# Optimization experiments

Measured on AMD Instinct MI355X. Metric: run time of the kernel, lower is better.

## Reference

```python
import jax, jax.numpy as jnp
import numpy as np
import math

B, L, DF = 1024, 96, 5
D_MODEL, D_FF, N_HEADS = 256, 1024, 8
C_OUT, MA, FACTOR = 5, 25, 3
E_LAYERS, D_LAYERS, EXT = 2, 2, 20


def moving_mean(x, k):
    # torch moving_avg: replicate-pad (k-1)//2 on each side, AvgPool1d(k, stride=1)
    p = (k - 1) // 2
    xp = jnp.concatenate([jnp.repeat(x[:, :1], p, axis=1), x, jnp.repeat(x[:, -1:], p, axis=1)], axis=1)
    cs = jnp.cumsum(xp, axis=1)
    cs = jnp.concatenate([jnp.zeros_like(cs[:, :1]), cs], axis=1)
    return (cs[:, k:] - cs[:, :-k]) / k


def series_decomp(x, k):
    m = moving_mean(x, k)
    return x - m, m


def circ_conv3(x, W):
    # Conv1d(kernel=3, padding=1, padding_mode='circular', bias=False); x (B,T,C), W (O,C,3)
    xp = jnp.pad(x, ((0, 0), (1, 1), (0, 0)), mode='wrap')
    win = jnp.stack([xp[:, :-2], xp[:, 1:-1], xp[:, 2:]], axis=-1)  # (B,T,C,3)
    return jnp.einsum('btct,oct->bto'.replace('btct', 'blct').replace('bto', 'blo'), win, W)


def my_layernorm(x, g, b):
    # LayerNorm over last dim, then subtract per-(batch,channel) seasonal bias (mean over time)
    mu = x.mean(-1, keepdims=True)
    var = ((x - mu) ** 2).mean(-1, keepdims=True)
    xh = (x - mu) / jnp.sqrt(var + 1e-5) * g + b
    return xh - xh.mean(axis=1, keepdims=True)


def time_delay_agg(values, corr):
    # inference-mode time delay aggregation; values, corr: (B,H,E,Lv)
    Bv, H, E, Lv = values.shape
    top_k = int(FACTOR * math.log(Lv))
    mean_value = corr.mean(axis=(1, 2))              # (B,Lv)
    weights, delay = jax.lax.top_k(mean_value, top_k)  # (B,k)
    tmp_corr = jax.nn.softmax(weights, axis=-1)
    ar = jnp.arange(Lv)

    def body(acc, wd):
        w, d = wd                                    # (B,), (B,) int32
        idx = (ar[None, :] + d[:, None]) % Lv        # circular roll == gather on doubled values
        pattern = jnp.take_along_axis(values, idx[:, None, None, :], axis=-1)
        return acc + pattern * w[:, None, None, None], None

    acc, _ = jax.lax.scan(body, jnp.zeros_like(values), (tmp_corr.T, delay.T))
    return acc


def auto_correlation(q, k, v):
    # q (B,Lq,H,E); k,v (B,S,H,E)
    Bq, Lq, H, E = q.shape
    S = v.shape[1]
    if Lq > S:
        pad = jnp.zeros((Bq, Lq - S, H, E), q.dtype)
        k = jnp.concatenate([k, pad], axis=1)
        v = jnp.concatenate([v, pad], axis=1)
    else:
        k, v = k[:, :Lq], v[:, :Lq]
    qf = jnp.fft.rfft(q.transpose(0, 2, 3, 1), axis=-1)
    kf = jnp.fft.rfft(k.transpose(0, 2, 3, 1), axis=-1)
    corr = jnp.fft.irfft(qf * jnp.conj(kf), n=Lq, axis=-1)  # (B,H,E,Lq)
    V = time_delay_agg(v.transpose(0, 2, 3, 1), corr)
    return V.transpose(0, 3, 1, 2)


def ac_layer(xq, xkv, Wq, bq, Wk, bk, Wv, bv, Wo, bo):
    Bq, Lq, _ = xq.shape
    S = xkv.shape[1]
    q = (xq @ Wq.T + bq).reshape(Bq, Lq, N_HEADS, -1)
    k = (xkv @ Wk.T + bk).reshape(Bq, S, N_HEADS, -1)
    v = (xkv @ Wv.T + bv).reshape(Bq, S, N_HEADS, -1)
    V = auto_correlation(q, k, v).reshape(Bq, Lq, -1)
    return V @ Wo.T + bo


def setup_inputs() -> dict:
    ks = iter(jax.random.split(jax.random.key(0), 64))

    def rn(shape, s=0.05):
        return jax.random.normal(next(ks), shape, jnp.float32) * s

    dm, E, D = D_MODEL, E_LAYERS, D_LAYERS
    inp = {'x': jax.random.normal(next(ks), (B, L, DF), jnp.float32)}
    inp['we_enc'] = rn((dm, DF, 3), 0.3)
    inp['we_dec'] = rn((dm, DF, 3), 0.3)
    for w in ('Wq', 'Wk', 'Wv', 'Wo'):
        inp['enc_' + w] = rn((E, dm, dm))
        inp['enc_b' + w[1]] = rn((E, dm))
    inp['enc_W1'] = rn((E, D_FF, dm))
    inp['enc_W2'] = rn((E, dm, D_FF))
    inp['enc_ln_g'] = jnp.ones((dm,), jnp.float32)
    inp['enc_ln_b'] = jnp.zeros((dm,), jnp.float32)
    for p in ('s', 'c'):
        for w in ('Wq', 'Wk', 'Wv', 'Wo'):
            inp['dec_' + p + w] = rn((D, dm, dm))
            inp['dec_' + p + 'b' + w[1]] = rn((D, dm))
    inp['dec_W1'] = rn((D, D_FF, dm))
    inp['dec_W2'] = rn((D, dm, D_FF))
    inp['dec_Wt'] = rn((D, C_OUT, dm, 3), 0.3)
    inp['dec_ln_g'] = jnp.ones((dm,), jnp.float32)
    inp['dec_ln_b'] = jnp.zeros((dm,), jnp.float32)
    inp['proj_W'] = rn((C_OUT, dm), 0.3)
    inp['proj_b'] = jnp.zeros((C_OUT,), jnp.float32)
    inp['bn_g'] = jnp.ones((EXT,), jnp.float32)
    inp['bn_b'] = jnp.zeros((EXT,), jnp.float32)
    inp['bn_rm'] = jnp.zeros((EXT,), jnp.float32)
    inp['bn_rv'] = jnp.ones((EXT,), jnp.float32)
    inp['fc_W'] = rn((1, EXT), 0.3)
    inp['fc_b'] = jnp.zeros((1,), jnp.float32)
    return inp


def reference(x, we_enc, we_dec,
              enc_Wq, enc_bq, enc_Wk, enc_bk, enc_Wv, enc_bv, enc_Wo, enc_bo,
              enc_W1, enc_W2, enc_ln_g, enc_ln_b,
              dec_sWq, dec_sbq, dec_sWk, dec_sbk, dec_sWv, dec_sbv, dec_sWo, dec_sbo,
              dec_cWq, dec_cbq, dec_cWk, dec_cbk, dec_cWv, dec_cbv, dec_cWo, dec_cbo,
              dec_W1, dec_W2, dec_Wt, dec_ln_g, dec_ln_b,
              proj_W, proj_b, bn_g, bn_b, bn_rm, bn_rv, fc_W, fc_b):
    mean = jnp.tile(x.mean(axis=1, keepdims=True), (1, EXT, 1))
    seasonal_init, trend_init = series_decomp(x, MA)
    trend_init = jnp.concatenate([trend_init, mean], axis=1)            # (B, L+EXT, DF)
    seasonal_init = jnp.pad(seasonal_init, ((0, 0), (EXT, 0), (0, 0)))  # 20 zero steps in front
    # encoder
    enc = circ_conv3(x, we_enc)  # DataEmbedding_wo_pos (dropout = identity in eval)
    for i in range(E_LAYERS):
        a = ac_layer(enc, enc, enc_Wq[i], enc_bq[i], enc_Wk[i], enc_bk[i],
                     enc_Wv[i], enc_bv[i], enc_Wo[i], enc_bo[i])
        h, _ = series_decomp(enc + a, MA)
        y = jax.nn.relu(h @ enc_W1[i].T) @ enc_W2[i].T  # 1x1 convs, bias=False
        enc, _ = series_decomp(h + y, MA)
    enc = my_layernorm(enc, enc_ln_g, enc_ln_b)
    # decoder
    dec = circ_conv3(seasonal_init, we_dec)
    trend = trend_init
    for i in range(D_LAYERS):
        a = ac_layer(dec, dec, dec_sWq[i], dec_sbq[i], dec_sWk[i], dec_sbk[i],
                     dec_sWv[i], dec_sbv[i], dec_sWo[i], dec_sbo[i])
        dec, t1 = series_decomp(dec + a, MA)
        a = ac_layer(dec, enc, dec_cWq[i], dec_cbq[i], dec_cWk[i], dec_cbk[i],
                     dec_cWv[i], dec_cbv[i], dec_cWo[i], dec_cbo[i])
        dec, t2 = series_decomp(dec + a, MA)
        y = jax.nn.relu(dec @ dec_W1[i].T) @ dec_W2[i].T
        dec, t3 = series_decomp(dec + y, MA)
        trend = trend + circ_conv3(t1 + t2 + t3, dec_Wt[i])
    dec = my_layernorm(dec, dec_ln_g, dec_ln_b)
    seasonal = dec @ proj_W.T + proj_b          # (B, L+EXT, C_OUT)
    seasonal = jnp.tile(seasonal, (1, 1, 4))    # (B, L+EXT, 20)
    out = jnp.tile(trend, (1, 1, 4)) + seasonal  # trend tiled to 20 channels (see notes)
    last = out[:, -1, :]                         # (B, 20)
    h = (last - bn_rm) / jnp.sqrt(bn_rv + 1e-5) * bn_g + bn_b  # BatchNorm1d eval
    return (h @ fc_W.T + fc_b)[:, 0]
```

## Files before the change

kernel.cpp:

```cpp
#include <hip/hip_runtime.h>
#include <hip/hip_bf16.h>
#include <cstdint>
#include <cstddef>

#define B_   1024
#define LE   96
#define LD   116
#define DM   256
#define DFF  1024

typedef __attribute__((ext_vector_type(8))) short bf16x8;
typedef __attribute__((ext_vector_type(4))) float f32x4;

static __device__ __forceinline__ unsigned short f2b(float f) {
  __hip_bfloat16 h = __float2bfloat16(f);
  return *reinterpret_cast<unsigned short*>(&h);
}
static __device__ __forceinline__ float asf(unsigned int u) { return __uint_as_float(u); }
static __device__ __forceinline__ void split1(float f, unsigned short& h, unsigned short& l) {
  h = f2b(f);
  l = f2b(f - asf((unsigned int)h << 16));
}
static __device__ __forceinline__ unsigned int pck(float f) {
  unsigned short h, l; split1(f, h, l);
  return ((unsigned int)h << 16) | l;
}
static __device__ __forceinline__ float unp(unsigned int p) {
  return asf(p & 0xFFFF0000u) + asf(p << 16);
}
static __device__ __forceinline__ void split8(float4 a, float4 b, uint4& h4, uint4& l4) {
  float f[8] = {a.x, a.y, a.z, a.w, b.x, b.y, b.z, b.w};
  unsigned int hp[4], lp[4];
#pragma unroll
  for (int j = 0; j < 4; ++j) {
    unsigned short h0, l0, h1, l1;
    split1(f[2 * j], h0, l0);
    split1(f[2 * j + 1], h1, l1);
    hp[j] = (unsigned int)h0 | ((unsigned int)h1 << 16);
    lp[j] = (unsigned int)l0 | ((unsigned int)l1 << 16);
  }
  h4 = make_uint4(hp[0], hp[1], hp[2], hp[3]);
  l4 = make_uint4(lp[0], lp[1], lp[2], lp[3]);
}
static __device__ __forceinline__ void unpack8(uint4 a, uint4 b, uint4& h, uint4& l) {
  h.x = (a.y & 0xFFFF0000u) | (a.x >> 16);
  l.x = (a.y << 16) | (a.x & 0xFFFFu);
  h.y = (a.w & 0xFFFF0000u) | (a.z >> 16);
  l.y = (a.w << 16) | (a.z & 0xFFFFu);
  h.z = (b.y & 0xFFFF0000u) | (b.x >> 16);
  l.z = (b.y << 16) | (b.x & 0xFFFFu);
  h.w = (b.w & 0xFFFF0000u) | (b.z >> 16);
  l.w = (b.w << 16) | (b.z & 0xFFFFu);
}

typedef const __attribute__((address_space(1))) void* gas_ptr;
typedef __attribute__((address_space(3))) void* las_ptr;
static __device__ __forceinline__ void gload16(const void* g, void* l) {
  __builtin_amdgcn_global_load_lds((gas_ptr)g, (las_ptr)l, 16, 0, 0);
}

#define NE_ ((size_t)B_ * LE * DM)
#define ND_ ((size_t)B_ * LD * DM)
#define NS_ ((size_t)B_ * LD * 5)
#define NW_ ((size_t)B_ * 16)
#define HID_ ((size_t)29696 * DFF)
#define WBF_ 3670016

static constexpr size_t o_enc   = 0;
static constexpr size_t o_dec   = o_enc   + NE_ * 4;
static constexpr size_t o_q     = o_dec   + ND_ * 4;
static constexpr size_t o_kbuf  = o_q     + ND_ * 4;
static constexpr size_t o_qkvp  = o_kbuf  + ND_ * 4;
static constexpr size_t o_qxp   = o_qkvp  + ND_ * 12;
static constexpr size_t o_ench  = o_qxp   + ND_ * 4;
static constexpr size_t o_encl  = o_ench  + NE_ * 2;
static constexpr size_t o_dech  = o_encl  + NE_ * 2;
static constexpr size_t o_decl  = o_dech  + ND_ * 2;
static constexpr size_t o_gthh  = o_decl  + ND_ * 2;
static constexpr size_t o_gthl  = o_gthh  + ND_ * 2;
static constexpr size_t o_hidp  = o_gthl  + ND_ * 2;
static constexpr size_t o_spad  = o_hidp  + HID_ * 4;
static constexpr size_t o_trend = o_spad  + NS_ * 4;
static constexpr size_t o_wtop  = o_trend + NS_ * 4;
static constexpr size_t o_dtop  = o_wtop  + NW_ * 4;
static constexpr size_t o_bias  = o_dtop  + NW_ * 4;
static constexpr size_t o_whi   = o_bias  + 6 * 768 * 4;
static constexpr size_t o_wlo   = o_whi   + (size_t)WBF_ * 2;
static constexpr size_t WS_TOTAL = o_wlo  + (size_t)WBF_ * 2;

__device__ __align__(256) unsigned char g_ws[WS_TOTAL];

static __host__ __device__ constexpr size_t enc_base(int i) { return (size_t)i * 786432; }
static __host__ __device__ constexpr size_t dec_base(int i) { return 1572864 + (size_t)i * 1048576; }

__global__ __launch_bounds__(256)
void k_cast_split(const float* __restrict__ in, unsigned short* __restrict__ hi,
                  unsigned short* __restrict__ lo, int n) {
  int i = (blockIdx.x * 256 + threadIdx.x) * 4;
  if (i < n) {
    float4 v = *(const float4*)(in + i);
    unsigned int hp[2], lp[2];
    float f[4] = {v.x, v.y, v.z, v.w};
#pragma unroll
    for (int j = 0; j < 2; ++j) {
      unsigned short h0, l0, h1, l1;
      split1(f[2 * j], h0, l0);
      split1(f[2 * j + 1], h1, l1);
      hp[j] = (unsigned int)h0 | ((unsigned int)h1 << 16);
      lp[j] = (unsigned int)l0 | ((unsigned int)l1 << 16);
    }
    *(uint2*)(hi + i) = make_uint2(hp[0], hp[1]);
    *(uint2*)(lo + i) = make_uint2(lp[0], lp[1]);
  }
}

__global__ __launch_bounds__(256)
void k_cat3(const float* __restrict__ a, const float* __restrict__ b,
            const float* __restrict__ c, float* __restrict__ dst) {
  int t = threadIdx.x;
  dst[t] = a[t];
  dst[256 + t] = b[t];
  if (c) dst[512 + t] = c[t];
}

__global__ __launch_bounds__(128)
void k_pre(const float* __restrict__ x, float* __restrict__ spad, float* __restrict__ trend) {
  int b = blockIdx.x;
  __shared__ float xs[LE * 5];
  __shared__ float mx[5];
  const float* xb = x + (size_t)b * LE * 5;
  for (int i = threadIdx.x; i < LE * 5; i += 128) xs[i] = xb[i];
  __syncthreads();
  if (threadIdx.x < 5) {
    float s = 0.f;
    for (int t = 0; t < LE; ++t) s += xs[t * 5 + threadIdx.x];
    mx[threadIdx.x] = s * (1.f / 96.f);
  }
  __syncthreads();
  float* spb = spad + (size_t)b * LD * 5;
  float* trb = trend + (size_t)b * LD * 5;
  for (int i = threadIdx.x; i < LE * 5; i += 128) {
    int t = i / 5, c = i % 5;
    float s = 0.f;
    for (int d = -12; d <= 12; ++d) {
      int tt = t + d; tt = tt < 0 ? 0 : (tt > LE - 1 ? LE - 1 : tt);
      s += xs[tt * 5 + c];
    }
    float m = s * (1.f / 25.f);
    trb[t * 5 + c] = m;
    spb[(t + 20) * 5 + c] = xs[i] - m;
  }
  for (int i = threadIdx.x; i < 20 * 5; i += 128) {
    int t = i / 5, c = i % 5;
    spb[t * 5 + c] = 0.f;
    trb[(LE + t) * 5 + c] = mx[c];
  }
}

__global__ __launch_bounds__(256)
void k_conv3(const float* __restrict__ xin, const float* __restrict__ W,
             float* __restrict__ out, unsigned short* __restrict__ ohi,
             unsigned short* __restrict__ olo, int L) {
  int b = blockIdx.x, o = threadIdx.x;
  __shared__ float xs[LD * 5];
  const float* xb = xin + (size_t)b * L * 5;
  for (int i = o; i < L * 5; i += 256) xs[i] = xb[i];
  __syncthreads();
  float w[15];
#pragma unroll
  for (int j = 0; j < 15; ++j) w[j] = W[o * 15 + j];
  size_t ob = (size_t)b * L * DM + o;
  for (int l = 0; l < L; ++l) {
    int lm = (l == 0) ? L - 1 : l - 1;
    int lp = (l == L - 1) ? 0 : l + 1;
    float acc = 0.f;
#pragma unroll
    for (int c = 0; c < 5; ++c)
      acc += xs[lm * 5 + c] * w[c * 3] + xs[l * 5 + c] * w[c * 3 + 1] + xs[lp * 5 + c] * w[c * 3 + 2];
    size_t gi = ob + (size_t)l * DM;
    out[gi] = acc;
    unsigned short h, lo2; split1(acc, h, lo2);
    ohi[gi] = h; olo[gi] = lo2;
  }
}

template <int XMODE, int OMODE, bool RELU>
__global__ __launch_bounds__(256)
void k_gemm_ps(const unsigned short* __restrict__ Xhi, const unsigned short* __restrict__ Xlo,
               const unsigned int* __restrict__ Xp,
               const unsigned short* __restrict__ Whi, const unsigned short* __restrict__ Wlo,
               const float* __restrict__ bias, float* __restrict__ Cf,
               unsigned int* __restrict__ Cp, int M, int N, int K) {
  __shared__ __align__(16) unsigned short Xh[4096], Xl[4096], Wh[4096], Wl[4096];
  const int nwg = gridDim.x, bid = blockIdx.x;
  const int wg = (bid & 7) * (nwg >> 3) + (bid >> 3);
  const int NT = N >> 7;
  const int mt = wg / NT, nt = wg % NT;
  const int m0 = mt << 7, n0 = nt << 7;
  const int tid = threadIdx.x, lane = tid & 63, wv = tid >> 6;
  const int wm = (wv >> 1) << 6, wn = (wv & 1) << 6;

  f32x4 acc[4][4];
#pragma unroll
  for (int i = 0; i < 4; ++i)
#pragma unroll
    for (int j = 0; j < 4; ++j) acc[i][j] = (f32x4){0.f, 0.f, 0.f, 0.f};

  const int r0 = tid >> 2,        ls0 = (tid & 3) ^ ((r0 >> 1) & 3);
  const int r1 = 64 + (tid >> 2), ls1 = (tid & 3) ^ ((r1 >> 1) & 3);
  const unsigned short* wh0 = Whi + (size_t)(n0 + r0) * K + (ls0 << 3);
  const unsigned short* wh1 = Whi + (size_t)(n0 + r1) * K + (ls1 << 3);
  const unsigned short* wl0 = Wlo + (size_t)(n0 + r0) * K + (ls0 << 3);
  const unsigned short* wl1 = Wlo + (size_t)(n0 + r1) * K + (ls1 << 3);
  const int lofs0 = (tid & ~63) << 3, lofs1 = 2048 + ((tid & ~63) << 3);

  const unsigned short* xh0 = nullptr; const unsigned short* xh1 = nullptr;
  const unsigned short* xl0 = nullptr; const unsigned short* xl1 = nullptr;
  const unsigned int* xp0 = nullptr; const unsigned int* xp1 = nullptr;
  unsigned short *xh0d = nullptr, *xl0d = nullptr, *xh1d = nullptr, *xl1d = nullptr;
  if (XMODE == 0) {
    xh0 = Xhi + (size_t)(m0 + r0) * K + (ls0 << 3);
    xh1 = Xhi + (size_t)(m0 + r1) * K + (ls1 << 3);
    xl0 = Xlo + (size_t)(m0 + r0) * K + (ls0 << 3);
    xl1 = Xlo + (size_t)(m0 + r1) * K + (ls1 << 3);
  } else {
    const int xrow0 = tid >> 2, xpart = tid & 3;
    const int xrow1 = 64 + xrow0;
    xp0 = Xp + (size_t)(m0 + xrow0) * K + (xpart << 3);
    xp1 = Xp + (size_t)(m0 + xrow1) * K + (xpart << 3);
    const int xph0 = xpart ^ ((xrow0 >> 1) & 3);
    const int xph1 = xpart ^ ((xrow1 >> 1) & 3);
    xh0d = Xh + xrow0 * 32 + (xph0 << 3);
    xl0d = Xl + xrow0 * 32 + (xph0 << 3);
    xh1d = Xh + xrow1 * 32 + (xph1 << 3);
    xl1d = Xl + xrow1 * 32 + (xph1 << 3);
  }

  for (int k0 = 0; k0 < K; k0 += 32) {
    gload16(wh0 + k0, Wh + lofs0);
    gload16(wh1 + k0, Wh + lofs1);
    gload16(wl0 + k0, Wl + lofs0);
    gload16(wl1 + k0, Wl + lofs1);
    if (XMODE == 0) {
      gload16(xh0 + k0, Xh + lofs0);
      gload16(xh1 + k0, Xh + lofs1);
      gload16(xl0 + k0, Xl + lofs0);
      gload16(xl1 + k0, Xl + lofs1);
    } else {
      uint4 a0 = *(const uint4*)(xp0 + k0);
      uint4 b0 = *(const uint4*)(xp0 + k0 + 4);
      uint4 a1 = *(const uint4*)(xp1 + k0);
      uint4 b1 = *(const uint4*)(xp1 + k0 + 4);
      uint4 h, l;
      unpack8(a0, b0, h, l);
      *(uint4*)xh0d = h; *(uint4*)xl0d = l;
      unpack8(a1, b1, h, l);
      *(uint4*)xh1d = h; *(uint4*)xl1d = l;
    }
    __syncthreads();
    bf16x8 ah[4], al[4], bh[4], bl[4];
#pragma unroll
    for (int i = 0; i < 4; ++i) {
      int ra = wm + i * 16 + (lane & 15);
      int sa = (lane >> 4) ^ ((ra >> 1) & 3);
      ah[i] = *(const bf16x8*)(Xh + ra * 32 + (sa << 3));
      al[i] = *(const bf16x8*)(Xl + ra * 32 + (sa << 3));
      int rb = wn + i * 16 + (lane & 15);
      int sb = (lane >> 4) ^ ((rb >> 1) & 3);
      bh[i] = *(const bf16x8*)(Wh + rb * 32 + (sb << 3));
      bl[i] = *(const bf16x8*)(Wl + rb * 32 + (sb << 3));
    }
#pragma unroll
    for (int i = 0; i < 4; ++i)
#pragma unroll
      for (int j = 0; j < 4; ++j) {
        acc[i][j] = __builtin_amdgcn_mfma_f32_16x16x32_bf16(ah[i], bh[j], acc[i][j], 0, 0, 0);
        acc[i][j] = __builtin_amdgcn_mfma_f32_16x16x32_bf16(al[i], bh[j], acc[i][j], 0, 0, 0);
        acc[i][j] = __builtin_amdgcn_mfma_f32_16x16x32_bf16(ah[i], bl[j], acc[i][j], 0, 0, 0);
      }
    __syncthreads();
  }
// ... 109 lines not shown

  float* vals = (float*)smem;
  float* rv   = vals + 128;
  int*   ri   = (int*)(rv + 128);
  float* selv = (float*)(ri + 128);
  int*   seli = (int*)(selv + 16);
  if (tid < 128) vals[tid] = (tid < L) ? s : -3e38f;
  __syncthreads();
  for (int it = 0; it < TK; ++it) {
    if (tid < 128) { rv[tid] = vals[tid]; ri[tid] = tid; }
    __syncthreads();
    for (int off = 64; off >= 1; off >>= 1) {
      if (tid < off) {
        float v2 = rv[tid + off]; int i2 = ri[tid + off];
        if (v2 > rv[tid] || (v2 == rv[tid] && i2 < ri[tid])) { rv[tid] = v2; ri[tid] = i2; }
      }
      __syncthreads();
    }
    if (tid == 0) { selv[it] = rv[0]; seli[it] = ri[0]; vals[ri[0]] = -3e38f; }
    __syncthreads();
  }
  if (tid == 0) {
    float mxv = selv[0];
    float e[16]; float sum = 0.f;
    for (int j = 0; j < TK; ++j) { e[j] = expf(selv[j] - mxv); sum += e[j]; }
    float inv = 1.f / sum;
    for (int j = 0; j < TK; ++j) {
      wout[(size_t)b * 16 + j] = e[j] * inv;
      dout[(size_t)b * 16 + j] = seli[j];
    }
  }
}

__global__ __launch_bounds__(256)
void k_gather4(const unsigned int* __restrict__ V, int sv, const float* __restrict__ wtop,
               const int* __restrict__ dtop, unsigned short* __restrict__ ohi,
               unsigned short* __restrict__ olo, int L, int S, int TK, int G8) {
  int p = blockIdx.x;
  int xcd = p & 7, q8 = p >> 3;
  int lg = q8 % G8;
  int b = ((q8 / G8) << 3) + xcd;
  __shared__ float wsm[16];
  __shared__ int   dsm[16];
  if (threadIdx.x < TK) {
    wsm[threadIdx.x] = wtop[(size_t)b * 16 + threadIdx.x];
    dsm[threadIdx.x] = dtop[(size_t)b * 16 + threadIdx.x];
  }
  __syncthreads();
  int wv = threadIdx.x >> 6, lane = threadIdx.x & 63;
  int c4 = lane << 2;
  const unsigned int* Vb = V + (size_t)b * S * sv + c4;
  size_t ob = (size_t)b * L * DM + c4;
#pragma unroll
  for (int u = 0; u < 2; ++u) {
    int l = (lg << 3) + (wv << 1) + u;
    if (l < L) {
      float a0 = 0.f, a1 = 0.f, a2 = 0.f, a3 = 0.f;
      for (int j = 0; j < TK; ++j) {
        int r = l + dsm[j]; if (r >= L) r -= L;
        if (r < S) {
          uint4 v = *(const uint4*)(Vb + (size_t)r * sv);
          float w = wsm[j];
          a0 += w * unp(v.x); a1 += w * unp(v.y); a2 += w * unp(v.z); a3 += w * unp(v.w);
        }
      }
      unsigned short h0, l0, h1, l1, h2, l2, h3, l3;
      split1(a0, h0, l0); split1(a1, h1, l1); split1(a2, h2, l2); split1(a3, h3, l3);
      uint2 hp, lp;
      hp.x = (unsigned int)h0 | ((unsigned int)h1 << 16);
      hp.y = (unsigned int)h2 | ((unsigned int)h3 << 16);
      lp.x = (unsigned int)l0 | ((unsigned int)l1 << 16);
      lp.y = (unsigned int)l2 | ((unsigned int)l3 << 16);
      *(uint2*)(ohi + ob + (size_t)l * DM) = hp;
      *(uint2*)(olo + ob + (size_t)l * DM) = lp;
    }
  }
}

template <int MOUT>
__global__ __launch_bounds__(128)
void k_decomp(const float* __restrict__ X, const float* __restrict__ Y,
              float* __restrict__ out, unsigned short* __restrict__ ohi,
              unsigned short* __restrict__ olo, float* __restrict__ mout, int L) {
  int b = blockIdx.x >> 2, qd = blockIdx.x & 3;
  __shared__ float tmp[LD * 64];
  size_t base = (size_t)b * L * DM + qd * 64;
  for (int i = threadIdx.x; i < L * 64; i += 128) {
    int t = i >> 6, cc = i & 63;
    size_t gi = base + (size_t)t * DM + cc;
    tmp[i] = X[gi] + Y[gi];
  }
  __syncthreads();
  int c = threadIdx.x & 63, th = threadIdx.x >> 6;
  int half = L >> 1;
  int t0 = th * half, t1 = t0 + half;
  float s = 0.f;
  for (int d = -12; d <= 12; ++d) {
    int t2 = t0 + d; t2 = t2 < 0 ? 0 : (t2 > L - 1 ? L - 1 : t2);
    s += tmp[t2 * 64 + c];
  }
  for (int t = t0; t < t1; ++t) {
    float m = s * (1.f / 25.f);
    size_t gi = base + (size_t)t * DM + c;
    float o = tmp[t * 64 + c] - m;
    out[gi] = o;
    unsigned short h, l; split1(o, h, l);
    ohi[gi] = h; olo[gi] = l;
    if (MOUT) mout[gi] = m;
    int ai = t + 13; if (ai > L - 1) ai = L - 1;
    int si = t - 12; if (si < 0) si = 0;
    s += tmp[ai * 64 + c] - tmp[si * 64 + c];
  }
}

__global__ __launch_bounds__(256)
void k_lnorm(const float* __restrict__ X, const float* __restrict__ g,
             float* __restrict__ out, unsigned short* __restrict__ ohi,
             unsigned short* __restrict__ olo, int L) {
  int b = blockIdx.x;
  __shared__ float mu_s[LD], inv_s[LD];
  size_t base = (size_t)b * L * DM;
  int wv = threadIdx.x >> 6, lane = threadIdx.x & 63;
  for (int t = wv; t < L; t += 4) {
    float s = 0.f, s2 = 0.f;
#pragma unroll
    for (int qd = 0; qd < 4; ++qd) {
      float val = X[base + (size_t)t * DM + lane + 64 * qd];
      s += val; s2 += val * val;
    }
    for (int off = 32; off; off >>= 1) { s += __shfl_xor(s, off); s2 += __shfl_xor(s2, off); }
    if (lane == 0) {
      float mu = s * (1.f / 256.f);
      mu_s[t] = mu;
      inv_s[t] = rsqrtf(s2 * (1.f / 256.f) - mu * mu + 1e-5f);
    }
  }
  __syncthreads();
  int c = threadIdx.x;
  float gc = g[c];
  float sm = 0.f;
  for (int t = 0; t < L; ++t) sm += (X[base + (size_t)t * DM + c] - mu_s[t]) * inv_s[t];
  float mn = sm / (float)L;
  for (int t = 0; t < L; ++t) {
    float xn = (X[base + (size_t)t * DM + c] - mu_s[t]) * inv_s[t];
    float o = gc * (xn - mn);
    size_t gi = base + (size_t)t * DM + c;
    out[gi] = o;
    unsigned short h, l; split1(o, h, l);
    ohi[gi] = h; olo[gi] = l;
  }
}

__global__ __launch_bounds__(256)
void k_trendconv(const float* __restrict__ T, const float* __restrict__ Wt,
                 float* __restrict__ trend, int L) {
  int b = blockIdx.x;
  int tid = threadIdx.x, wv = tid >> 6, lane = tid & 63;
  int c0 = lane << 2;
  float w[5][3][4];
#pragma unroll
  for (int o = 0; o < 5; ++o)
#pragma unroll
    for (int k = 0; k < 4; ++k) {
      w[o][0][k] = Wt[o * 768 + (c0 + k) * 3 + 0];
      w[o][1][k] = Wt[o * 768 + (c0 + k) * 3 + 1];
      w[o][2][k] = Wt[o * 768 + (c0 + k) * 3 + 2];
    }
  size_t base = (size_t)b * L * DM;
  int chunk = (L + 3) >> 2;
  int l0 = wv * chunk;
  int cnt = (L - l0 < chunk) ? (L - l0) : chunk;
  if (cnt <= 0) return;
  int lmi = (l0 == 0) ? L - 1 : l0 - 1;
  float4 pm = *(const float4*)(T + base + (size_t)lmi * DM + c0);
  float4 p0 = *(const float4*)(T + base + (size_t)l0  * DM + c0);
  for (int i = 0; i < cnt; ++i) {
    int l = l0 + i;
    int lp = (l == L - 1) ? 0 : l + 1;
    float4 pp = *(const float4*)(T + base + (size_t)lp * DM + c0);
    float fm[4] = {pm.x, pm.y, pm.z, pm.w};
    float f0[4] = {p0.x, p0.y, p0.z, p0.w};
    float fp[4] = {pp.x, pp.y, pp.z, pp.w};
// ... 63 lines not shown
  const float* enc_bk = (const float*)d_in[6];
  const float* enc_Wv = (const float*)d_in[7];
  const float* enc_bv = (const float*)d_in[8];
  const float* enc_Wo = (const float*)d_in[9];
  const float* enc_bo = (const float*)d_in[10];
  const float* enc_W1 = (const float*)d_in[11];
  const float* enc_W2 = (const float*)d_in[12];
  const float* enc_g  = (const float*)d_in[13];
  const float* sWq = (const float*)d_in[15]; const float* sbq = (const float*)d_in[16];
  const float* sWk = (const float*)d_in[17]; const float* sbk = (const float*)d_in[18];
  const float* sWv = (const float*)d_in[19]; const float* sbv = (const float*)d_in[20];
  const float* sWo = (const float*)d_in[21]; const float* sbo = (const float*)d_in[22];
  const float* cWq = (const float*)d_in[23]; const float* cbq = (const float*)d_in[24];
  const float* cWk = (const float*)d_in[25]; const float* cbk = (const float*)d_in[26];
  const float* cWv = (const float*)d_in[27]; const float* cbv = (const float*)d_in[28];
  const float* cWo = (const float*)d_in[29]; const float* cbo = (const float*)d_in[30];
  const float* dW1 = (const float*)d_in[31]; const float* dW2 = (const float*)d_in[32];
  const float* dWt = (const float*)d_in[33];
  const float* dec_g  = (const float*)d_in[34];
  const float* projW = (const float*)d_in[36]; const float* projb = (const float*)d_in[37];
  const float* bng = (const float*)d_in[38]; const float* bnb = (const float*)d_in[39];
  const float* bnrm = (const float*)d_in[40]; const float* bnrv = (const float*)d_in[41];
  const float* fcW = (const float*)d_in[42]; const float* fcb = (const float*)d_in[43];
  (void)in_sizes; (void)n_in; (void)out_size; (void)d_ws; (void)ws_size;
  float* outp = (float*)d_out;

  void* symaddr = nullptr;
  if (hipGetSymbolAddress(&symaddr, HIP_SYMBOL(g_ws)) != hipSuccess || !symaddr) return;
  unsigned char* base = (unsigned char*)symaddr;
  float* enc   = (float*)(base + o_enc);
  float* dec   = (float*)(base + o_dec);
  float* q     = (float*)(base + o_q);
  float* kbuf  = (float*)(base + o_kbuf);
  unsigned int* qkvp = (unsigned int*)(base + o_qkvp);
  unsigned int* qxp  = (unsigned int*)(base + o_qxp);
  unsigned short* ench = (unsigned short*)(base + o_ench);
  unsigned short* encl = (unsigned short*)(base + o_encl);
  unsigned short* dech = (unsigned short*)(base + o_dech);
  unsigned short* decl = (unsigned short*)(base + o_decl);
  unsigned short* gthh = (unsigned short*)(base + o_gthh);
  unsigned short* gthl = (unsigned short*)(base + o_gthl);
  unsigned int*   hidp = (unsigned int*)(base + o_hidp);
  float* spad  = (float*)(base + o_spad);
  float* trend = (float*)(base + o_trend);
  float* wtop  = (float*)(base + o_wtop);
  int*   dtop  = (int*)(base + o_dtop);
  float* biasb = (float*)(base + o_bias);
  unsigned short* whi = (unsigned short*)(base + o_whi);
  unsigned short* wlo = (unsigned short*)(base + o_wlo);

  const int ME = B_ * LE;
  const int MD = B_ * LD;

  auto cast = [&](const float* s, size_t off, int n) {
    k_cast_split<<<n / 1024, 256, 0, stream>>>(s, whi + off, wlo + off, n);
  };
  for (int i = 0; i < 2; ++i) {
    size_t e = enc_base(i), d = dec_base(i);
    size_t wq = (size_t)i * 65536, wf = (size_t)i * 262144;
    cast(enc_Wq + wq, e + 0, 65536);       cast(enc_Wk + wq, e + 65536, 65536);
    cast(enc_Wv + wq, e + 131072, 65536);  cast(enc_Wo + wq, e + 196608, 65536);
    cast(enc_W1 + wf, e + 262144, 262144); cast(enc_W2 + wf, e + 524288, 262144);
    cast(sWq + wq, d + 0, 65536);          cast(sWk + wq, d + 65536, 65536);
    cast(sWv + wq, d + 131072, 65536);     cast(sWo + wq, d + 196608, 65536);
    cast(cWq + wq, d + 262144, 65536);     cast(cWk + wq, d + 327680, 65536);
    cast(cWv + wq, d + 393216, 65536);     cast(cWo + wq, d + 458752, 65536);
    cast(dW1 + wf, d + 524288, 262144);    cast(dW2 + wf, d + 786432, 262144);
    size_t b_ = (size_t)i * DM;
    k_cat3<<<1, 256, 0, stream>>>(enc_bq + b_, enc_bk + b_, enc_bv + b_, biasb + (size_t)i * 768);
    k_cat3<<<1, 256, 0, stream>>>(sbq + b_, sbk + b_, sbv + b_, biasb + (size_t)(2 + i) * 768);
    k_cat3<<<1, 256, 0, stream>>>(cbk + b_, cbv + b_, nullptr, biasb + (size_t)(4 + i) * 768);
  }

  auto gemm_f = [&](const unsigned short* Xh, const unsigned short* Xl, size_t woff,
                    const float* bias, float* Cf, int M, int N, int K) {
    int nwg = (M >> 7) * (N >> 7);
    k_gemm_ps<0, 0, false><<<nwg, 256, 0, stream>>>(Xh, Xl, nullptr, whi + woff, wlo + woff,
                                                    bias, Cf, nullptr, M, N, K);
  };
  auto gemm_p = [&](const unsigned short* Xh, const unsigned short* Xl, size_t woff,
                    const float* bias, unsigned int* Cp, int M, int N, int K) {
    int nwg = (M >> 7) * (N >> 7);
    k_gemm_ps<0, 1, false><<<nwg, 256, 0, stream>>>(Xh, Xl, nullptr, whi + woff, wlo + woff,
                                                    bias, nullptr, Cp, M, N, K);
  };
  auto ffn = [&](const unsigned short* srch, const unsigned short* srcl, int M,
                 size_t w1, size_t w2) {
    int done = 0;
    while (done < M) {
      int mc = (M - done < 29696) ? (M - done) : 29696;
      int nwg1 = (mc >> 7) * (DFF >> 7);
      k_gemm_ps<0, 1, true><<<nwg1, 256, 0, stream>>>(srch + (size_t)done * DM,
                                                      srcl + (size_t)done * DM, nullptr,
                                                      whi + w1, wlo + w1, nullptr,
                                                      nullptr, hidp, mc, DFF, DM);
      int nwg2 = (mc >> 7) * (DM >> 7);
      k_gemm_ps<1, 0, false><<<nwg2, 256, 0, stream>>>(nullptr, nullptr, hidp,
                                                       whi + w2, wlo + w2, nullptr,
                                                       kbuf + (size_t)done * DM, nullptr,
                                                       mc, DM, DFF);
      done += mc;
    }
  };
  auto attn_self = [&](const unsigned short* srch, const unsigned short* srcl, int Lq,
                       size_t wqkv, size_t wo2, const float* biasr, const float* bo, int TK) {
    int M = B_ * Lq;
    int G8 = (Lq + 7) >> 3;
    gemm_p(srch, srcl, wqkv, biasr, qkvp, M, 768, DM);
    k_corr_split<<<B_, 256, 0, stream>>>(qkvp, 768, qkvp + 256, 768, wtop, dtop, Lq, Lq, TK);
    k_gather4<<<B_ * G8, 256, 0, stream>>>(qkvp + 512, 768, wtop, dtop, gthh, gthl, Lq, Lq, TK, G8);
    gemm_f(gthh, gthl, wo2, bo, q, M, DM, DM);
  };
  auto attn_cross = [&](size_t wq2, size_t wkv, size_t wo2, const float* bq,
                        const float* biasr, const float* bo, int TK) {
    int G8 = (LD + 7) >> 3;
    gemm_p(dech, decl, wq2, bq, qxp, MD, DM, DM);
    gemm_p(ench, encl, wkv, biasr, qkvp, ME, 512, DM);
    k_corr_split<<<B_, 256, 0, stream>>>(qxp, 256, qkvp, 512, wtop, dtop, LD, LE, TK);
    k_gather4<<<B_ * G8, 256, 0, stream>>>(qkvp + 256, 512, wtop, dtop, gthh, gthl, LD, LE, TK, G8);
    gemm_f(gthh, gthl, wo2, bo, q, MD, DM, DM);
  };

  k_pre<<<B_, 128, 0, stream>>>(x, spad, trend);
  k_conv3<<<B_, 256, 0, stream>>>(x, we_enc, enc, ench, encl, LE);
  k_conv3<<<B_, 256, 0, stream>>>(spad, we_dec, dec, dech, decl, LD);

  for (int i = 0; i < 2; ++i) {
    size_t e = enc_base(i), b_ = (size_t)i * DM;
    attn_self(ench, encl, LE, e + 0, e + 196608, biasb + (size_t)i * 768, enc_bo + b_, 13);
    k_decomp<0><<<4 * B_, 128, 0, stream>>>(enc, q, enc, ench, encl, nullptr, LE);
    ffn(ench, encl, ME, e + 262144, e + 524288);
    k_decomp<0><<<4 * B_, 128, 0, stream>>>(enc, kbuf, enc, ench, encl, nullptr, LE);
  }
  k_lnorm<<<B_, 256, 0, stream>>>(enc, enc_g, enc, ench, encl, LE);

  for (int i = 0; i < 2; ++i) {
    size_t d = dec_base(i), b_ = (size_t)i * DM;
    const float* Wt_i = dWt + (size_t)i * 5 * DM * 3;
    attn_self(dech, decl, LD, d + 0, d + 196608, biasb + (size_t)(2 + i) * 768, sbo + b_, 14);
    k_decomp<1><<<4 * B_, 128, 0, stream>>>(dec, q, dec, dech, decl, kbuf, LD);
    k_trendconv<<<B_, 256, 0, stream>>>(kbuf, Wt_i, trend, LD);
    attn_cross(d + 262144, d + 327680, d + 458752, cbq + b_, biasb + (size_t)(4 + i) * 768, cbo + b_, 14);
    k_decomp<1><<<4 * B_, 128, 0, stream>>>(dec, q, dec, dech, decl, kbuf, LD);
    k_trendconv<<<B_, 256, 0, stream>>>(kbuf, Wt_i, trend, LD);
    ffn(dech, decl, MD, d + 524288, d + 786432);
    k_decomp<1><<<4 * B_, 128, 0, stream>>>(dec, kbuf, dec, dech, decl, q, LD);
    k_trendconv<<<B_, 256, 0, stream>>>(q, Wt_i, trend, LD);
  }
  k_lnorm<<<B_, 256, 0, stream>>>(dec, dec_g, dec, dech, decl, LD);

  k_final<<<B_, 256, 0, stream>>>(dec, trend, projW, projb, bng, bnb, bnrm, bnrv, fcW, fcb, outp);
}
```

Baseline: 6.477 ms.

## Fold Wq·Wk and Wo·Wv into composed weights for self-attention, pack activations

For self-attention, correlation is computed from X·(WkᵀWq) against the raw input, and the value path uses a precomposed Wo·Wv, so the separate Q/K projection and output GEMM are dropped; the gather writes the final float output with a folded bias. Activations are stored as packed hi/lo uint32 everywhere instead of separate hi/lo arrays, so the GEMM has a single input mode. The FFN hidden buffer is enlarged so it runs unchunked. Dropping the Q/K biases and composing the weights in split-bf16 changes rounding and relies on the correlation being bilinear in Q and K.

```diff
diff --git a/kernel.cpp b/kernel.cpp
--- a/kernel.cpp
+++ b/kernel.cpp
@@ -27,20 +27,6 @@
 }
 static __device__ __forceinline__ float unp(unsigned int p) {
   return asf(p & 0xFFFF0000u) + asf(p << 16);
-}
-static __device__ __forceinline__ void split8(float4 a, float4 b, uint4& h4, uint4& l4) {
-  float f[8] = {a.x, a.y, a.z, a.w, b.x, b.y, b.z, b.w};
-  unsigned int hp[4], lp[4];
-#pragma unroll
-  for (int j = 0; j < 4; ++j) {
-    unsigned short h0, l0, h1, l1;
-    split1(f[2 * j], h0, l0);
-    split1(f[2 * j + 1], h1, l1);
-    hp[j] = (unsigned int)h0 | ((unsigned int)h1 << 16);
-    lp[j] = (unsigned int)l0 | ((unsigned int)l1 << 16);
-  }
-  h4 = make_uint4(hp[0], hp[1], hp[2], hp[3]);
-  l4 = make_uint4(lp[0], lp[1], lp[2], lp[3]);
 }
 static __device__ __forceinline__ void unpack8(uint4 a, uint4 b, uint4& h, uint4& l) {
   h.x = (a.y & 0xFFFF0000u) | (a.x >> 16);
@@ -63,35 +49,31 @@
 #define ND_ ((size_t)B_ * LD * DM)
 #define NS_ ((size_t)B_ * LD * 5)
 #define NW_ ((size_t)B_ * 16)
-#define HID_ ((size_t)29696 * DFF)
-#define WBF_ 3670016
+#define WBF_ 3145728
 
 static constexpr size_t o_enc   = 0;
 static constexpr size_t o_dec   = o_enc   + NE_ * 4;
 static constexpr size_t o_q     = o_dec   + ND_ * 4;
 static constexpr size_t o_kbuf  = o_q     + ND_ * 4;
-static constexpr size_t o_qkvp  = o_kbuf  + ND_ * 4;
-static constexpr size_t o_qxp   = o_qkvp  + ND_ * 12;
-static constexpr size_t o_ench  = o_qxp   + ND_ * 4;
-static constexpr size_t o_encl  = o_ench  + NE_ * 2;
-static constexpr size_t o_dech  = o_encl  + NE_ * 2;
-static constexpr size_t o_decl  = o_dech  + ND_ * 2;
-static constexpr size_t o_gthh  = o_decl  + ND_ * 2;
-static constexpr size_t o_gthl  = o_gthh  + ND_ * 2;
-static constexpr size_t o_hidp  = o_gthl  + ND_ * 2;
-static constexpr size_t o_spad  = o_hidp  + HID_ * 4;
+static constexpr size_t o_yup   = o_kbuf  + ND_ * 4;
+static constexpr size_t o_qxp   = o_yup   + ND_ * 8;
+static constexpr size_t o_encp  = o_qxp   + ND_ * 4;
+static constexpr size_t o_decp  = o_encp  + NE_ * 4;
+static constexpr size_t o_gthp  = o_decp  + ND_ * 4;
+static constexpr size_t o_hidp  = o_gthp  + ND_ * 4;
+static constexpr size_t o_spad  = o_hidp  + ND_ * 16;
 static constexpr size_t o_trend = o_spad  + NS_ * 4;
 static constexpr size_t o_wtop  = o_trend + NS_ * 4;
 static constexpr size_t o_dtop  = o_wtop  + NW_ * 4;
 static constexpr size_t o_bias  = o_dtop  + NW_ * 4;
-static constexpr size_t o_whi   = o_bias  + 6 * 768 * 4;
+static constexpr size_t o_whi   = o_bias  + 2048 * 4;
 static constexpr size_t o_wlo   = o_whi   + (size_t)WBF_ * 2;
 static constexpr size_t WS_TOTAL = o_wlo  + (size_t)WBF_ * 2;
 
 __device__ __align__(256) unsigned char g_ws[WS_TOTAL];
 
-static __host__ __device__ constexpr size_t enc_base(int i) { return (size_t)i * 786432; }
-static __host__ __device__ constexpr size_t dec_base(int i) { return 1572864 + (size_t)i * 1048576; }
+static __host__ __device__ constexpr size_t enc_base(int i) { return (size_t)i * 655360; }
+static __host__ __device__ constexpr size_t dec_base(int i) { return 1310720 + (size_t)i * 917504; }
 
 __global__ __launch_bounds__(256)
 void k_cast_split(const float* __restrict__ in, unsigned short* __restrict__ hi,
@@ -115,12 +97,46 @@
 }
 
 __global__ __launch_bounds__(256)
-void k_cat3(const float* __restrict__ a, const float* __restrict__ b,
-            const float* __restrict__ c, float* __restrict__ dst) {
+void k_compose_qk(const float* __restrict__ Wq, const float* __restrict__ Wk,
+                  unsigned short* __restrict__ hi, unsigned short* __restrict__ lo) {
+  int j = blockIdx.x, i = threadIdx.x;
+  __shared__ float wkc[256];
+  wkc[i] = Wk[i * 256 + j];
+  __syncthreads();
+  float s = 0.f;
+  for (int o = 0; o < 256; ++o) s += Wq[o * 256 + i] * wkc[o];
+  unsigned short h, l; split1(s, h, l);
+  hi[j * 256 + i] = h; lo[j * 256 + i] = l;
+}
+__global__ __launch_bounds__(256)
+void k_compose_vo(const float* __restrict__ Wv, const float* __restrict__ Wo,
+                  unsigned short* __restrict__ hi, unsigned short* __restrict__ lo) {
+  int o2 = blockIdx.x, i = threadIdx.x;
+  __shared__ float woc[256];
+  woc[i] = Wo[o2 * 256 + i];
+  __syncthreads();
+  float s = 0.f;
+  for (int c = 0; c < 256; ++c) s += woc[c] * Wv[c * 256 + i];
+  unsigned short h, l; split1(s, h, l);
+  hi[o2 * 256 + i] = h; lo[o2 * 256 + i] = l;
+}
+__global__ __launch_bounds__(256)
+void k_bout(const float* __restrict__ Wo, const float* __restrict__ bv,
+            const float* __restrict__ bo, float* __restrict__ dst) {
+  int o2 = threadIdx.x;
+  __shared__ float bvs[256];
+  bvs[o2] = bv[o2];
+  __syncthreads();
+  float s = bo[o2];
+  for (int c = 0; c < 256; ++c) s += Wo[o2 * 256 + c] * bvs[c];
+  dst[o2] = s;
+}
+
+__global__ __launch_bounds__(256)
+void k_cat2(const float* __restrict__ a, const float* __restrict__ b, float* __restrict__ dst) {
   int t = threadIdx.x;
   dst[t] = a[t];
   dst[256 + t] = b[t];
-  if (c) dst[512 + t] = c[t];
 }
 
 __global__ __launch_bounds__(128)
@@ -159,8 +175,7 @@
 
 __global__ __launch_bounds__(256)
 void k_conv3(const float* __restrict__ xin, const float* __restrict__ W,
-             float* __restrict__ out, unsigned short* __restrict__ ohi,
-             unsigned short* __restrict__ olo, int L) {
+             float* __restrict__ out, unsigned int* __restrict__ shp, int L) {
   int b = blockIdx.x, o = threadIdx.x;
   __shared__ float xs[LD * 5];
   const float* xb = xin + (size_t)b * L * 5;
@@ -179,15 +194,13 @@
       acc += xs[lm * 5 + c] * w[c * 3] + xs[l * 5 + c] * w[c * 3 + 1] + xs[lp * 5 + c] * w[c * 3 + 2];
     size_t gi = ob + (size_t)l * DM;
     out[gi] = acc;
-    unsigned short h, lo2; split1(acc, h, lo2);
-    ohi[gi] = h; olo[gi] = lo2;
-  }
-}
-
-template <int XMODE, int OMODE, bool RELU>
-__global__ __launch_bounds__(256)
-void k_gemm_ps(const unsigned short* __restrict__ Xhi, const unsigned short* __restrict__ Xlo,
-               const unsigned int* __restrict__ Xp,
+    shp[gi] = pck(acc);
+  }
+}
+
+template <int OMODE, bool RELU>
+__global__ __launch_bounds__(256)
+void k_gemm_pk(const unsigned int* __restrict__ Xp,
                const unsigned short* __restrict__ Whi, const unsigned short* __restrict__ Wlo,
                const float* __restrict__ bias, float* __restrict__ Cf,
                unsigned int* __restrict__ Cp, int M, int N, int K) {
@@ -214,39 +227,23 @@
   const unsigned short* wl1 = Wlo + (size_t)(n0 + r1) * K + (ls1 << 3);
   const int lofs0 = (tid & ~63) << 3, lofs1 = 2048 + ((tid & ~63) << 3);
 
-  const unsigned short* xh0 = nullptr; const unsigned short* xh1 = nullptr;
-  const unsigned short* xl0 = nullptr; const unsigned short* xl1 = nullptr;
-  const unsigned int* xp0 = nullptr; const unsigned int* xp1 = nullptr;
-  unsigned short *xh0d = nullptr, *xl0d = nullptr, *xh1d = nullptr, *xl1d = nullptr;
-  if (XMODE == 0) {
-    xh0 = Xhi + (size_t)(m0 + r0) * K + (ls0 << 3);
-    xh1 = Xhi + (size_t)(m0 + r1) * K + (ls1 << 3);
-    xl0 = Xlo + (size_t)(m0 + r0) * K + (ls0 << 3);
-    xl1 = Xlo + (size_t)(m0 + r1) * K + (ls1 << 3);
-  } else {
-    const int xrow0 = tid >> 2, xpart = tid & 3;
-    const int xrow1 = 64 + xrow0;
-    xp0 = Xp + (size_t)(m0 + xrow0) * K + (xpart << 3);
-    xp1 = Xp + (size_t)(m0 + xrow1) * K + (xpart << 3);
-    const int xph0 = xpart ^ ((xrow0 >> 1) & 3);
-    const int xph1 = xpart ^ ((xrow1 >> 1) & 3);
-    xh0d = Xh + xrow0 * 32 + (xph0 << 3);
-    xl0d = Xl + xrow0 * 32 + (xph0 << 3);
-    xh1d = Xh + xrow1 * 32 + (xph1 << 3);
-    xl1d = Xl + xrow1 * 32 + (xph1 << 3);
-  }
+  const int xrow0 = tid >> 2, xpart = tid & 3;
+  const int xrow1 = 64 + xrow0;
+  const unsigned int* xp0 = Xp + (size_t)(m0 + xrow0) * K + (xpart << 3);
+  const unsigned int* xp1 = Xp + (size_t)(m0 + xrow1) * K + (xpart << 3);
+  const int xph0 = xpart ^ ((xrow0 >> 1) & 3);
+  const int xph1 = xpart ^ ((xrow1 >> 1) & 3);
+  unsigned short* xh0d = Xh + xrow0 * 32 + (xph0 << 3);
+  unsigned short* xl0d = Xl + xrow0 * 32 + (xph0 << 3);
+  unsigned short* xh1d = Xh + xrow1 * 32 + (xph1 << 3);
+  unsigned short* xl1d = Xl + xrow1 * 32 + (xph1 << 3);
 
   for (int k0 = 0; k0 < K; k0 += 32) {
     gload16(wh0 + k0, Wh + lofs0);
     gload16(wh1 + k0, Wh + lofs1);
     gload16(wl0 + k0, Wl + lofs0);
     gload16(wl1 + k0, Wl + lofs1);
-    if (XMODE == 0) {
-      gload16(xh0 + k0, Xh + lofs0);
-      gload16(xh1 + k0, Xh + lofs1);
-      gload16(xl0 + k0, Xl + lofs0);
-      gload16(xl1 + k0, Xl + lofs1);
-    } else {
+    {
       uint4 a0 = *(const uint4*)(xp0 + k0);
       uint4 b0 = *(const uint4*)(xp0 + k0 + 4);
       uint4 a1 = *(const uint4*)(xp1 + k0);
@@ -422,20 +419,24 @@
   }
 }
 
-__global__ __launch_bounds__(256)
-void k_gather4(const unsigned int* __restrict__ V, int sv, const float* __restrict__ wtop,
-               const int* __restrict__ dtop, unsigned short* __restrict__ ohi,
-               unsigned short* __restrict__ olo, int L, int S, int TK, int G8) {
+template <int SELF>
+__global__ __launch_bounds__(256)
+void k_gather5(const unsigned int* __restrict__ V, int sv, const float* __restrict__ wtop,
+               const int* __restrict__ dtop, float* __restrict__ outf,
+               unsigned int* __restrict__ outp, const float* __restrict__ bout,
+               int L, int S, int TK, int G8) {
   int p = blockIdx.x;
   int xcd = p & 7, q8 = p >> 3;
   int lg = q8 % G8;
   int b = ((q8 / G8) << 3) + xcd;
   __shared__ float wsm[16];
   __shared__ int   dsm[16];
+  __shared__ float bsm[256];
   if (threadIdx.x < TK) {
     wsm[threadIdx.x] = wtop[(size_t)b * 16 + threadIdx.x];
     dsm[threadIdx.x] = dtop[(size_t)b * 16 + threadIdx.x];
   }
+  if (SELF) bsm[threadIdx.x] = bout[threadIdx.x];
   __syncthreads();
   int wv = threadIdx.x >> 6, lane = threadIdx.x & 63;
   int c4 = lane << 2;
@@ -454,15 +455,15 @@
           a0 += w * unp(v.x); a1 += w * unp(v.y); a2 += w * unp(v.z); a3 += w * unp(v.w);
         }
       }
-      unsigned short h0, l0, h1, l1, h2, l2, h3, l3;
-      split1(a0, h0, l0); split1(a1, h1, l1); split1(a2, h2, l2); split1(a3, h3, l3);
-      uint2 hp, lp;
-      hp.x = (unsigned int)h0 | ((unsigned int)h1 << 16);
-      hp.y = (unsigned int)h2 | ((unsigned int)h3 << 16);
-      lp.x = (unsigned int)l0 | ((unsigned int)l1 << 16);
-      lp.y = (unsigned int)l2 | ((unsigned int)l3 << 16);
-      *(uint2*)(ohi + ob + (size_t)l * DM) = hp;
-      *(uint2*)(olo + ob + (size_t)l * DM) = lp;
+      if (SELF) {
+        float4 o;
+        o.x = a0 + bsm[c4];     o.y = a1 + bsm[c4 + 1];
+        o.z = a2 + bsm[c4 + 2]; o.w = a3 + bsm[c4 + 3];
+        *(float4*)(outf + ob + (size_t)l * DM) = o;
+      } else {
+        uint4 o; o.x = pck(a0); o.y = pck(a1); o.z = pck(a2); o.w = pck(a3);
+        *(uint4*)(outp + ob + (size_t)l * DM) = o;
+      }
     }
   }
 }
@@ -470,8 +471,8 @@
 template <int MOUT>
 __global__ __launch_bounds__(128)
 void k_decomp(const float* __restrict__ X, const float* __restrict__ Y,
-              float* __restrict__ out, unsigned short* __restrict__ ohi,
-              unsigned short* __restrict__ olo, float* __restrict__ mout, int L) {
+              float* __restrict__ out, unsigned int* __restrict__ shp,
+              float* __restrict__ mout, int L) {
   int b = blockIdx.x >> 2, qd = blockIdx.x & 3;
   __shared__ float tmp[LD * 64];
   size_t base = (size_t)b * L * DM + qd * 64;
@@ -494,8 +495,7 @@
     size_t gi = base + (size_t)t * DM + c;
     float o = tmp[t * 64 + c] - m;
     out[gi] = o;
-    unsigned short h, l; split1(o, h, l);
-    ohi[gi] = h; olo[gi] = l;
+    shp[gi] = pck(o);
     if (MOUT) mout[gi] = m;
     int ai = t + 13; if (ai > L - 1) ai = L - 1;
     int si = t - 12; if (si < 0) si = 0;
@@ -505,8 +505,7 @@
 
 __global__ __launch_bounds__(256)
 void k_lnorm(const float* __restrict__ X, const float* __restrict__ g,
-             float* __restrict__ out, unsigned short* __restrict__ ohi,
-             unsigned short* __restrict__ olo, int L) {
+             float* __restrict__ out, unsigned int* __restrict__ shp, int L) {
   int b = blockIdx.x;
   __shared__ float mu_s[LD], inv_s[LD];
   size_t base = (size_t)b * L * DM;
@@ -536,8 +535,7 @@
     float o = gc * (xn - mn);
     size_t gi = base + (size_t)t * DM + c;
     out[gi] = o;
-    unsigned short h, l; split1(o, h, l);
-    ohi[gi] = h; olo[gi] = l;
+    shp[gi] = pck(o);
   }
 }
 
@@ -667,15 +665,12 @@
   float* dec   = (float*)(base + o_dec);
   float* q     = (float*)(base + o_q);
   float* kbuf  = (float*)(base + o_kbuf);
-  unsigned int* qkvp = (unsigned int*)(base + o_qkvp);
+  unsigned int* yup  = (unsigned int*)(base + o_yup);
   unsigned int* qxp  = (unsigned int*)(base + o_qxp);
-  unsigned short* ench = (unsigned short*)(base + o_ench);
-  unsigned short* encl = (unsigned short*)(base + o_encl);
-  unsigned short* dech = (unsigned short*)(base + o_dech);
-  unsigned short* decl = (unsigned short*)(base + o_decl);
-  unsigned short* gthh = (unsigned short*)(base + o_gthh);
-  unsigned short* gthl = (unsigned short*)(base + o_gthl);
-  unsigned int*   hidp = (unsigned int*)(base + o_hidp);
+  unsigned int* encp = (unsigned int*)(base + o_encp);
+  unsigned int* decp = (unsigned int*)(base + o_decp);
+  unsigned int* gthp = (unsigned int*)(base + o_gthp);
+  unsigned int* hidp = (unsigned int*)(base + o_hidp);
   float* spad  = (float*)(base + o_spad);
   float* trend = (float*)(base + o_trend);
   float* wtop  = (float*)(base + o_wtop);
@@ -693,96 +688,84 @@
   for (int i = 0; i < 2; ++i) {
     size_t e = enc_base(i), d = dec_base(i);
     size_t wq = (size_t)i * 65536, wf = (size_t)i * 262144;
-    cast(enc_Wq + wq, e + 0, 65536);       cast(enc_Wk + wq, e + 65536, 65536);
-    cast(enc_Wv + wq, e + 131072, 65536);  cast(enc_Wo + wq, e + 196608, 65536);
-    cast(enc_W1 + wf, e + 262144, 262144); cast(enc_W2 + wf, e + 524288, 262144);
-    cast(sWq + wq, d + 0, 65536);          cast(sWk + wq, d + 65536, 65536);
-    cast(sWv + wq, d + 131072, 65536);     cast(sWo + wq, d + 196608, 65536);
-    cast(cWq + wq, d + 262144, 65536);     cast(cWk + wq, d + 327680, 65536);
-    cast(cWv + wq, d + 393216, 65536);     cast(cWo + wq, d + 458752, 65536);
-    cast(dW1 + wf, d + 524288, 262144);    cast(dW2 + wf, d + 786432, 262144);
     size_t b_ = (size_t)i * DM;
-    k_cat3<<<1, 256, 0, stream>>>(enc_bq + b_, enc_bk + b_, enc_bv + b_, biasb + (size_t)i * 768);
-    k_cat3<<<1, 256, 0, stream>>>(sbq + b_, sbk + b_, sbv + b_, biasb + (size_t)(2 + i) * 768);
-    k_cat3<<<1, 256, 0, stream>>>(cbk + b_, cbv + b_, nullptr, biasb + (size_t)(4 + i) * 768);
-  }
-
-  auto gemm_f = [&](const unsigned short* Xh, const unsigned short* Xl, size_t woff,
-                    const float* bias, float* Cf, int M, int N, int K) {
+    k_compose_qk<<<256, 256, 0, stream>>>(enc_Wq + wq, enc_Wk + wq, whi + e, wlo + e);
+    k_compose_vo<<<256, 256, 0, stream>>>(enc_Wv + wq, enc_Wo + wq, whi + e + 65536, wlo + e + 65536);
+    k_bout<<<1, 256, 0, stream>>>(enc_Wo + wq, enc_bv + b_, enc_bo + b_, biasb + (size_t)i * 256);
+    cast(enc_W1 + wf, e + 131072, 262144);
+    cast(enc_W2 + wf, e + 393216, 262144);
+    k_compose_qk<<<256, 256, 0, stream>>>(sWq + wq, sWk + wq, whi + d, wlo + d);
+    k_compose_vo<<<256, 256, 0, stream>>>(sWv + wq, sWo + wq, whi + d + 65536, wlo + d + 65536);
+    k_bout<<<1, 256, 0, stream>>>(sWo + wq, sbv + b_, sbo + b_, biasb + (size_t)(2 + i) * 256);
+    cast(cWq + wq, d + 131072, 65536);
+    cast(cWk + wq, d + 196608, 65536);
+    cast(cWv + wq, d + 262144, 65536);
+    cast(cWo + wq, d + 327680, 65536);
+    cast(dW1 + wf, d + 393216, 262144);
+    cast(dW2 + wf, d + 655360, 262144);
+    k_cat2<<<1, 256, 0, stream>>>(cbk + b_, cbv + b_, biasb + 1024 + (size_t)i * 512);
+  }
+
+  auto gemm_f = [&](const unsigned int* Xp, size_t woff, const float* bias, float* Cf,
+                    int M, int N, int K) {
     int nwg = (M >> 7) * (N >> 7);
-    k_gemm_ps<0, 0, false><<<nwg, 256, 0, stream>>>(Xh, Xl, nullptr, whi + woff, wlo + woff,
-                                                    bias, Cf, nullptr, M, N, K);
+    k_gemm_pk<0, false><<<nwg, 256, 0, stream>>>(Xp, whi + woff, wlo + woff, bias, Cf, nullptr, M, N, K);
   };
-  auto gemm_p = [&](const unsigned short* Xh, const unsigned short* Xl, size_t woff,
-                    const float* bias, unsigned int* Cp, int M, int N, int K) {
+  auto gemm_p = [&](const unsigned int* Xp, size_t woff, const float* bias, unsigned int* Cp,
+                    int M, int N, int K, bool relu) {
     int nwg = (M >> 7) * (N >> 7);
-    k_gemm_ps<0, 1, false><<<nwg, 256, 0, stream>>>(Xh, Xl, nullptr, whi + woff, wlo + woff,
-                                                    bias, nullptr, Cp, M, N, K);
+    if (relu) k_gemm_pk<1, true ><<<nwg, 256, 0, stream>>>(Xp, whi + woff, wlo + woff, bias, nullptr, Cp, M, N, K);
+    else      k_gemm_pk<1, false><<<nwg, 256, 0, stream>>>(Xp, whi + woff, wlo + woff, bias, nullptr, Cp, M, N, K);
   };
-  auto ffn = [&](const unsigned short* srch, const unsigned short* srcl, int M,
-                 size_t w1, size_t w2) {
-    int done = 0;
-    while (done < M) {
-      int mc = (M - done < 29696) ? (M - done) : 29696;
-      int nwg1 = (mc >> 7) * (DFF >> 7);
-      k_gemm_ps<0, 1, true><<<nwg1, 256, 0, stream>>>(srch + (size_t)done * DM,
-                                                      srcl + (size_t)done * DM, nullptr,
-                                                      whi + w1, wlo + w1, nullptr,
-                                                      nullptr, hidp, mc, DFF, DM);
-      int nwg2 = (mc >> 7) * (DM >> 7);
-      k_gemm_ps<1, 0, false><<<nwg2, 256, 0, stream>>>(nullptr, nullptr, hidp,
-                                                       whi + w2, wlo + w2, nullptr,
-                                                       kbuf + (size_t)done * DM, nullptr,
-                                                       mc, DM, DFF);
-      done += mc;
-    }
+  auto ffn = [&](const unsigned int* srcp, int M, size_t w1, size_t w2) {
+    gemm_p(srcp, w1, nullptr, hidp, M, DFF, DM, true);
+    gemm_f(hidp, w2, nullptr, kbuf, M, DM, DFF);
   };
-  auto attn_self = [&](const unsigned short* srch, const unsigned short* srcl, int Lq,
-                       size_t wqkv, size_t wo2, const float* biasr, const float* bo, int TK) {
+  auto attn_self = [&](const unsigned int* srcp, int Lq, size_t wyu, const float* bout, int TK) {
     int M = B_ * Lq;
     int G8 = (Lq + 7) >> 3;
-    gemm_p(srch, srcl, wqkv, biasr, qkvp, M, 768, DM);
-    k_corr_split<<<B_, 256, 0, stream>>>(qkvp, 768, qkvp + 256, 768, wtop, dtop, Lq, Lq, TK);
-    k_gather4<<<B_ * G8, 256, 0, stream>>>(qkvp + 512, 768, wtop, dtop, gthh, gthl, Lq, Lq, TK, G8);
-    gemm_f(gthh, gthl, wo2, bo, q, M, DM, DM);
+    gemm_p(srcp, wyu, nullptr, yup, M, 512, DM, false);
+    k_corr_split<<<B_, 256, 0, stream>>>(yup, 512, srcp, 256, wtop, dtop, Lq, Lq, TK);
+    k_gather5<1><<<B_ * G8, 256, 0, stream>>>(yup + 256, 512, wtop, dtop, q, nullptr, bout, Lq, Lq, TK, G8);
   };
   auto attn_cross = [&](size_t wq2, size_t wkv, size_t wo2, const float* bq,
-                        const float* biasr, const float* bo, int TK) {
+                        const float* bkv, const float* bo, int TK) {
     int G8 = (LD + 7) >> 3;
-    gemm_p(dech, decl, wq2, bq, qxp, MD, DM, DM);
-    gemm_p(ench, encl, wkv, biasr, qkvp, ME, 512, DM);
-    k_corr_split<<<B_, 256, 0, stream>>>(qxp, 256, qkvp, 512, wtop, dtop, LD, LE, TK);
-    k_gather4<<<B_ * G8, 256, 0, stream>>>(qkvp + 256, 512, wtop, dtop, gthh, gthl, LD, LE, TK, G8);
-    gemm_f(gthh, gthl, wo2, bo, q, MD, DM, DM);
+    gemm_p(decp, wq2, bq, qxp, MD, DM, DM, false);
+    gemm_p(encp, wkv, bkv, yup, ME, 512, DM, false);
+    k_corr_split<<<B_, 256, 0, stream>>>(qxp, 256, yup, 512, wtop, dtop, LD, LE, TK);
+    k_gather5<0><<<B_ * G8, 256, 0, stream>>>(yup + 256, 512, wtop, dtop, nullptr, gthp, nullptr, LD, LE, TK, G8);
+    gemm_f(gthp, wo2, bo, q, MD, DM, DM);
   };
 
   k_pre<<<B_, 128, 0, stream>>>(x, spad, trend);
-  k_conv3<<<B_, 256, 0, stream>>>(x, we_enc, enc, ench, encl, LE);
-  k_conv3<<<B_, 256, 0, stream>>>(spad, we_dec, dec, dech, decl, LD);
+  k_conv3<<<B_, 256, 0, stream>>>(x, we_enc, enc, encp, LE);
+  k_conv3<<<B_, 256, 0, stream>>>(spad, we_dec, dec, decp, LD);
 
   for (int i = 0; i < 2; ++i) {
-    size_t e = enc_base(i), b_ = (size_t)i * DM;
-    attn_self(ench, encl, LE, e + 0, e + 196608, biasb + (size_t)i * 768, enc_bo + b_, 13);
-    k_decomp<0><<<4 * B_, 128, 0, stream>>>(enc, q, enc, ench, encl, nullptr, LE);
-    ffn(ench, encl, ME, e + 262144, e + 524288);
-    k_decomp<0><<<4 * B_, 128, 0, stream>>>(enc, kbuf, enc, ench, encl, nullptr, LE);
-  }
-  k_lnorm<<<B_, 256, 0, stream>>>(enc, enc_g, enc, ench, encl, LE);
+    size_t e = enc_base(i);
+    attn_self(encp, LE, e + 0, biasb + (size_t)i * 256, 13);
+    k_decomp<0><<<4 * B_, 128, 0, stream>>>(enc, q, enc, encp, nullptr, LE);
+    ffn(encp, ME, e + 131072, e + 393216);
+    k_decomp<0><<<4 * B_, 128, 0, stream>>>(enc, kbuf, enc, encp, nullptr, LE);
+  }
+  k_lnorm<<<B_, 256, 0, stream>>>(enc, enc_g, enc, encp, LE);
 
   for (int i = 0; i < 2; ++i) {
-    size_t d = dec_base(i), b_ = (size_t)i * DM;
+    size_t d = dec_base(i);
+    size_t b_ = (size_t)i * DM;
     const float* Wt_i = dWt + (size_t)i * 5 * DM * 3;
-    attn_self(dech, decl, LD, d + 0, d + 196608, biasb + (size_t)(2 + i) * 768, sbo + b_, 14);
-    k_decomp<1><<<4 * B_, 128, 0, stream>>>(dec, q, dec, dech, decl, kbuf, LD);
+    attn_self(decp, LD, d + 0, biasb + (size_t)(2 + i) * 256, 14);
+    k_decomp<1><<<4 * B_, 128, 0, stream>>>(dec, q, dec, decp, kbuf, LD);
     k_trendconv<<<B_, 256, 0, stream>>>(kbuf, Wt_i, trend, LD);
-    attn_cross(d + 262144, d + 327680, d + 458752, cbq + b_, biasb + (size_t)(4 + i) * 768, cbo + b_, 14);
-    k_decomp<1><<<4 * B_, 128, 0, stream>>>(dec, q, dec, dech, decl, kbuf, LD);
+    attn_cross(d + 131072, d + 196608, d + 327680, cbq + b_, biasb + 1024 + (size_t)i * 512, cbo + b_, 14);
+    k_decomp<1><<<4 * B_, 128, 0, stream>>>(dec, q, dec, decp, kbuf, LD);
     k_trendconv<<<B_, 256, 0, stream>>>(kbuf, Wt_i, trend, LD);
-    ffn(dech, decl, MD, d + 524288, d + 786432);
-    k_decomp<1><<<4 * B_, 128, 0, stream>>>(dec, kbuf, dec, dech, decl, q, LD);
+    ffn(decp, MD, d + 393216, d + 655360);
+    k_decomp<1><<<4 * B_, 128, 0, stream>>>(dec, kbuf, dec, decp, q, LD);
     k_trendconv<<<B_, 256, 0, stream>>>(q, Wt_i, trend, LD);
   }
-  k_lnorm<<<B_, 256, 0, stream>>>(dec, dec_g, dec, dech, decl, LD);
+  k_lnorm<<<B_, 256, 0, stream>>>(dec, dec_g, dec, decp, LD);
 
   k_final<<<B_, 256, 0, stream>>>(dec, trend, projW, projb, bng, bnb, bnrm, bnrv, fcW, fcb, outp);
 }
```

New measurement: 6.149 ms. 1.05x faster.
